# Performance work log

Measured on AMD Instinct MI355X. Metric: run time of the kernel, lower is better.

The kernel has to match this reference:

```python
import jax, jax.numpy as jnp
import numpy as np
import math

B, S, U, H = 8, 1024, 1024, 16
DK = U // H  # 64


def setup_inputs() -> dict:
    key = jax.random.key(0)
    ks = jax.random.split(key, 12)
    query = jax.random.normal(ks[0], (B, S, U), jnp.float32)
    key_t = jax.random.normal(ks[1], (B, S, U), jnp.float32)  # unused by module (bug preserved)
    value = jax.random.normal(ks[2], (B, S, U), jnp.float32)  # unused by module (bug preserved)
    # causal multiplicative 0/1 mask [B,S,S]
    mask = jnp.broadcast_to(jnp.tril(jnp.ones((S, S), jnp.float32)), (B, S, S))
    bh = math.sqrt(1.0 / DK)   # init bound for per-head projections (out_features=d_k)
    bo = math.sqrt(1.0 / U)    # init bound for output projection (out_features=n_units)
    u = lambda k, shape, b: jax.random.uniform(k, shape, jnp.float32, -b, b)
    # per-head weights stacked: [H, U, DK] (already input->output layout)
    Wq = u(ks[3], (H, U, DK), bh); bq = u(ks[4], (H, DK), bh)
    Wk = u(ks[5], (H, U, DK), bh); bk = u(ks[6], (H, DK), bh)
    Wv = u(ks[7], (H, U, DK), bh); bv = u(ks[8], (H, DK), bh)
    Wo = u(ks[9], (U, U), bo);     bo_ = u(ks[10], (U,), bo)
    return dict(query=query, key=key_t, value=value, mask=mask,
                Wq=Wq, bq=bq, Wk=Wk, bk=bk, Wv=Wv, bv=bv, Wo=Wo, bo=bo_)


def reference(query, key, value, mask, Wq, bq, Wk, bk, Wv, bv, Wo, bo):
    # NOTE: faithful to source — q, k, v are ALL projected from `query`.
    q = jnp.einsum('bsu,hud->bhsd', query, Wq) + bq[:, None, :]
    k = jnp.einsum('bsu,hud->bhsd', query, Wk) + bk[:, None, :]
    v = jnp.einsum('bsu,hud->bhsd', query, Wv) + bv[:, None, :]
    scores = jnp.einsum('bhqd,bhkd->bhqk', q, k) / math.sqrt(DK)
    s = mask[:, None, :, :]  # broadcast over heads
    x = scores * s - 1e9 * (1.0 - s)  # multiplicative mask baked into softmax input
    attn = jax.nn.softmax(x, axis=-1)
    out = jnp.einsum('bhqk,bhkd->bhqd', attn, v)
    # concat heads along feature dim (head 0 first, matching torch.cat order)
    out = out.transpose(0, 2, 1, 3).reshape(B, S, U)
    return out @ Wo + bo
```

## Files before the change

### kernel.cpp

```cpp
#include <hip/hip_runtime.h>
#include <hip/hip_bf16.h>

#define B_ 8
#define S_ 1024
#define U_ 1024
#define H_ 16
#define DK_ 64

typedef __attribute__((ext_vector_type(8))) short short8;
typedef __attribute__((ext_vector_type(4))) float f32x4;
typedef __attribute__((ext_vector_type(16))) float f32x16;

__device__ inline ushort f2b(float x) {
  union { float f; unsigned u; } v; v.f = x;
  unsigned r = (v.u + 0x7FFFu + ((v.u >> 16) & 1u)) >> 16;
  return (ushort)r;
}
__device__ inline unsigned pk2(float lo, float hi) {
  return (unsigned)f2b(lo) | ((unsigned)f2b(hi) << 16);
}

__device__ inline void gld16(const ushort* g, ushort* l) {
  __builtin_amdgcn_global_load_lds((__attribute__((address_space(1))) void*)(g),
                                   (__attribute__((address_space(3))) void*)(l),
                                   16, 0, 0);
}

__global__ __launch_bounds__(256) void pack_all_kern(
    const float* __restrict__ X, ushort* __restrict__ Xb,
    const float* __restrict__ Wq, const float* __restrict__ Wk, const float* __restrict__ Wv,
    const float* __restrict__ bq, const float* __restrict__ bk, const float* __restrict__ bv,
    const float* __restrict__ Wo,
    ushort* __restrict__ Wqkv, float* __restrict__ Bqkv, ushort* __restrict__ Wob)
{
  __shared__ ushort tile[64*65];
  const int t = threadIdx.x;
  if (blockIdx.x < 4096) {
    int idx = blockIdx.x * 256 + t;
    const float4* src = (const float4*)X + (size_t)idx * 2;
    float4 a = src[0], b = src[1];
    ushort r[8];
    r[0]=f2b(a.x); r[1]=f2b(a.y); r[2]=f2b(a.z); r[3]=f2b(a.w);
    r[4]=f2b(b.x); r[5]=f2b(b.y); r[6]=f2b(b.z); r[7]=f2b(b.w);
    *(uint4*)(Xb + (size_t)idx*8) = *(uint4*)r;
    return;
  }
  const int bid = blockIdx.x - 4096;
  if (bid < 768) {
    int p = bid >> 8, rem = bid & 255;
    int h = rem >> 4, kc = rem & 15, k0 = kc*64;
    const float* Wsrc = (p==0) ? Wq : ((p==1) ? Wk : Wv);
    #pragma unroll
    for (int i = 0; i < 16; ++i) {
      int e = t + i*256;
      int r = e >> 6, d = e & 63;
      tile[d*65 + r] = f2b(Wsrc[h*65536 + (k0+r)*64 + d]);
    }
    __syncthreads();
    #pragma unroll
    for (int i = 0; i < 16; ++i) {
      int e = t + i*256;
      int d = e >> 6, r = e & 63;
      Wqkv[(size_t)(p*1024 + h*64 + d)*1024 + k0 + r] = tile[d*65 + r];
    }
    if (kc == 0 && t < 64) {
      const float* bsrc = (p==0) ? bq : ((p==1) ? bk : bv);
      Bqkv[p*1024 + h*64 + t] = bsrc[h*64 + t];
    }
  } else {
    int b2 = bid - 768;
    int nc = b2 >> 4, kc = b2 & 15;
    int n0 = nc*64, k0 = kc*64;
    #pragma unroll
    for (int i = 0; i < 16; ++i) {
      int e = t + i*256;
      int r = e >> 6, d = e & 63;
      tile[d*65 + r] = f2b(Wo[(size_t)(k0+r)*1024 + n0 + d]);
    }
    __syncthreads();
    #pragma unroll
    for (int i = 0; i < 16; ++i) {
      int e = t + i*256;
      int d = e >> 6, r = e & 63;
      Wob[(size_t)(n0+d)*1024 + k0 + r] = tile[d*65 + r];
    }
  }
}

template<int MODE>
__global__ __launch_bounds__(256, 3) void gemm128_kern(
    const ushort* __restrict__ A,
    const ushort* __restrict__ Bw,
    const float* __restrict__ bias,
    ushort* __restrict__ Qb, ushort* __restrict__ Kb, ushort* __restrict__ Vtb,
    float* __restrict__ outF)
{
  __shared__ __align__(16) ushort As[3][4096];
  __shared__ __align__(16) ushort Bs[3][4096];

  const int t = threadIdx.x;
  const int l = t & 63, w = t >> 6;
  const int wr = w >> 1, wc = w & 1;
  const int li = l & 15, c4 = l >> 4;

  int m0, n0;
  if (MODE==0) {
    int swz = (blockIdx.x & 7) * 192 + (blockIdx.x >> 3);
    int ms = swz / 192, rem = swz % 192;
    m0 = (ms*8 + (rem & 7)) * 128;  n0 = (rem >> 3) * 128;
  } else {
    int swz = (blockIdx.x & 7) * 64 + (blockIdx.x >> 3);
    int ms = swz / 64, rem = swz % 64;
    m0 = (ms*8 + (rem & 7)) * 128;  n0 = (rem >> 3) * 128;
  }

  f32x4 acc[4][4];
  #pragma unroll
  for (int i=0;i<4;i++)
    #pragma unroll
    for (int j=0;j<4;j++) acc[i][j] = (f32x4)0.0f;

  auto SA = [&](int buf, int kk) {
    #pragma unroll
    for (int p2=0;p2<2;++p2) {
      int n = p2*256 + t;
      int row = n >> 2, jj = (n & 3) ^ ((row >> 1) & 3);
      gld16(&A[(size_t)(m0 + row)*1024 + kk + jj*8], &As[buf][n*8]);
    }
  };
  auto SB = [&](int buf, int kk) {
    #pragma unroll
    for (int p2=0;p2<2;++p2) {
      int n = p2*256 + t;
      int row = n >> 2, jj = (n & 3) ^ ((row >> 1) & 3);
      gld16(&Bw[(size_t)(n0 + row)*1024 + kk + jj*8], &Bs[buf][n*8]);
    }
  };

  SA(0, 0);  SB(0, 0);
  SA(1, 32); SB(1, 32);

  for (int kt = 0; kt < 32; ++kt) {
    const int cur = kt % 3;
    asm volatile("s_waitcnt vmcnt(4)" ::: "memory");
    __builtin_amdgcn_s_barrier();
    __builtin_amdgcn_sched_barrier(0);

    short8 af[4], bf[4];
    #pragma unroll
    for (int i=0;i<4;i++) {
      int rA = wr*64 + i*16 + li;
      int rB = wc*64 + i*16 + li;
      af[i] = *(const short8*)&As[cur][rA*32 + ((c4 ^ ((rA>>1)&3))*8)];
      bf[i] = *(const short8*)&Bs[cur][rB*32 + ((c4 ^ ((rB>>1)&3))*8)];
    }
    __builtin_amdgcn_s_barrier();
    __builtin_amdgcn_sched_barrier(0);
    const int nb = (kt + 2) % 3;
    const int kk2 = ((kt + 2) & 31) * 32;
    SA(nb, kk2); SB(nb, kk2);

    __builtin_amdgcn_s_setprio(1);
    #pragma unroll
    for (int i=0;i<4;i++)
      #pragma unroll
      for (int j=0;j<4;j++)
        acc[i][j] = __builtin_amdgcn_mfma_f32_16x16x32_bf16(af[i], bf[j], acc[i][j], 0,0,0);
    __builtin_amdgcn_s_setprio(0);
  }

  #pragma unroll
  for (int i=0;i<4;i++) {
    int rbase = m0 + wr*64 + i*16 + c4*4;
    #pragma unroll
    for (int j=0;j<4;j++) {
      int col = n0 + wc*64 + j*16 + li;
      float bv = bias[col];
      if (MODE == 0) {
        int p = col >> 10, h = (col >> 6) & 15, d = col & 63;
        int b = rbase >> 10, s = rbase & 1023;
        if (p == 2) {
          ushort pk4[4];
          #pragma unroll
          for (int r=0;r<4;r++) pk4[r] = f2b(acc[i][j][r] + bv);
          *(uint2*)&Vtb[((size_t)((b*16+h)*64 + d))*1024 + s] = *(uint2*)pk4;
        } else {
          ushort* dst = (p==0) ? Qb : Kb;
          float sc = (p==0) ? 0.18033688011112042f : 1.0f;
          #pragma unroll
          for (int r=0;r<4;r++)
            dst[(((size_t)(b*16 + h))*1024 + s + r)*64 + d] = f2b((acc[i][j][r] + bv) * sc);
        }
      } else {
        #pragma unroll
        for (int r=0;r<4;r++)
          outF[(size_t)(rbase+r)*1024 + col] = acc[i][j][r] + bv;
      }
    }
  }
}

__global__ __launch_bounds__(256, 2) void attn_kern(
    const ushort* __restrict__ Qb, const ushort* __restrict__ Kb,
    const ushort* __restrict__ Vt, ushort* __restrict__ Ob)
{
  __shared__ __align__(16) ushort Pb[4][32*40];
  __shared__ __align__(16) ushort OT[4][32*72];
  const int t = threadIdx.x, l = t & 63, w = t >> 6;
  const int bid = blockIdx.x;
  const int x = bid & 7, i0 = bid >> 3;
  const int bh = x*16 + (i0 >> 2);
  const int p  = (i0 & 3)*4 + w;
  const int qta = p, qtb = 31 - p;

  const int col = l & 31, hi = l >> 5;
  const ushort* Qp = Qb + (size_t)bh*65536;
  const ushort* Kp = Kb + (size_t)bh*65536;
  const ushort* Vp = Vt + (size_t)bh*65536;

  short8 qfa[4], qfb[4];
  #pragma unroll
  for (int m=0;m<4;m++) {
    qfa[m] = *(const short8*)&Qp[(size_t)(qta*32+col)*64 + m*16 + hi*8];
    qfb[m] = *(const short8*)&Qp[(size_t)(qtb*32+col)*64 + m*16 + hi*8];
  }

  f32x16 aA0 = (f32x16)0.0f, aA1 = (f32x16)0.0f;
  f32x16 aB0 = (f32x16)0.0f, aB1 = (f32x16)0.0f;
  float mA = -1e30f, lA = 0.0f, mB = -1e30f, lB = 0.0f;
  ushort* Pw = &Pb[w][0];

  auto PROC = [&](f32x16& s, bool diag, float& mR, float& lS,
                  f32x16& o0, f32x16& o1, const short8* vf0, const short8* vf1) {
    if (diag) {
      #pragma unroll
      for (int r=0;r<16;r++) {
        int kvl = (r&3) + ((r>>2)<<3) + 4*hi;
        s[r] = (kvl > col) ? -1e9f : s[r];
      }
    }
    float mx = s[0];
    #pragma unroll
    for (int r=1;r<16;r++) mx = fmaxf(mx, s[r]);
    mx = fmaxf(mx, __shfl_xor(mx, 32));
    if (__any(mx - mR > 8.0f)) {
      float mN = fmaxf(mR, mx);
      float corr = __builtin_amdgcn_exp2f(mR - mN);
      mR = mN; lS *= corr;
      #pragma unroll
      for (int r=0;r<16;r++) { o0[r] *= corr; o1[r] *= corr; }
    }
    float pr[16], rs = 0.0f;
    #pragma unroll
    for (int r=0;r<16;r++) { pr[r] = __builtin_amdgcn_exp2f(s[r] - mR); rs += pr[r]; }
    rs += __shfl_xor(rs, 32);
    lS += rs;
    #pragma unroll
    for (int r2=0;r2<8;r2++) {
      int r = 2*r2;
      int kv = (r&3) + ((r>>2)<<3) + 4*hi;
      *(unsigned*)&Pw[col*40 + kv] = pk2(pr[r], pr[r+1]);
    }
    short8 pb0 = *(const short8*)&Pw[col*40 + hi*8];
    short8 pb1 = *(const short8*)&Pw[col*40 + 16 + hi*8];
    o0 = __builtin_amdgcn_mfma_f32_32x32x16_bf16(vf0[0], pb0, o0, 0,0,0);
    o0 = __builtin_amdgcn_mfma_f32_32x32x16_bf16(vf0[1], pb1, o0, 0,0,0);
    o1 = __builtin_amdgcn_mfma_f32_32x32x16_bf16(vf1[0], pb0, o1, 0,0,0);
    o1 = __builtin_amdgcn_mfma_f32_32x32x16_bf16(vf1[1], pb1, o1, 0,0,0);
  };

  auto LOADKV = [&](int kt, short8* kf_, short8* v0_, short8* v1_) {
    #pragma unroll
    for (int m=0;m<4;m++)
      kf_[m] = *(const short8*)&Kp[(size_t)(kt*32+col)*64 + m*16 + hi*8];
    #pragma unroll
    for (int m=0;m<2;m++) {
      v0_[m] = *(const short8*)&Vp[(size_t)col*1024      + kt*32 + m*16 + hi*8];
      v1_[m] = *(const short8*)&Vp[(size_t)(32+col)*1024 + kt*32 + m*16 + hi*8];
    }
  };

  short8 kf[4], vf0[2], vf1[2];
  LOADKV(0, kf, vf0, vf1);

  for (int kt = 0; kt <= qtb; ++kt) {
    short8 kf2[4], v02[2], v12[2];
    const int ktn = (kt + 1 <= qtb) ? kt + 1 : qtb;
    LOADKV(ktn, kf2, v02, v12);

    const bool doA = (kt <= qta);
    f32x16 sB = (f32x16)0.0f, sA = (f32x16)0.0f;
    #pragma unroll
    for (int m=0;m<4;m++)
      sB = __builtin_amdgcn_mfma_f32_32x32x16_bf16(kf[m], qfb[m], sB, 0, 0, 0);
    if (doA) {
      #pragma unroll
      for (int m=0;m<4;m++)
        sA = __builtin_amdgcn_mfma_f32_32x32x16_bf16(kf[m], qfa[m], sA, 0, 0, 0);
    }

    PROC(sB, kt == qtb, mB, lB, aB0, aB1, vf0, vf1);
    if (doA) PROC(sA, kt == qta, mA, lA, aA0, aA1, vf0, vf1);

    #pragma unroll
    for (int m=0;m<4;m++) kf[m] = kf2[m];
    #pragma unroll
    for (int m=0;m<2;m++) { vf0[m] = v02[m]; vf1[m] = v12[m]; }
  }

  const int b = bh >> 4, h = bh & 15;
  auto EPI = [&](int qt, float lS, const f32x16& o0, const f32x16& o1) {
    float inv = 1.0f / lS;
    ushort* o = &OT[w][0];
    #pragma unroll
    for (int r2=0;r2<8;r2++) {
      int r = 2*r2;
      int dv = (r&3) + ((r>>2)<<3) + 4*hi;
      *(unsigned*)&o[col*72 + dv]      = pk2(o0[r]*inv, o0[r+1]*inv);
      *(unsigned*)&o[col*72 + 32 + dv] = pk2(o1[r]*inv, o1[r+1]*inv);
    }
    #pragma unroll
    for (int it=0; it<4; ++it) {
      int q = it*8 + (l>>3), c8 = (l&7)*8;
      uint4 v = *(const uint4*)&o[q*72 + c8];
      int qg = qt*32 + q;
      *(uint4*)&Ob[(size_t)(b*1024+qg)*1024 + h*64 + c8] = v;
    }
  };
  EPI(qta, lA, aA0, aA1);
  EPI(qtb, lB, aB0, aB1);
}

extern "C" void kernel_launch(void* const* d_in, const int* in_sizes, int n_in,
                              void* d_out, int out_size, void* d_ws, size_t ws_size,
                              hipStream_t stream) {
  const float* query = (const float*)d_in[0];
  const float* Wq = (const float*)d_in[4];
  const float* bq = (const float*)d_in[5];
  const float* Wk = (const float*)d_in[6];
  const float* bk = (const float*)d_in[7];
  const float* Wv = (const float*)d_in[8];
  const float* bv = (const float*)d_in[9];
  const float* Wo = (const float*)d_in[10];
  const float* bo = (const float*)d_in[11];

  char* wsb = (char*)d_ws;
  ushort* Xb   = (ushort*)(wsb);
  ushort* Wqkv = (ushort*)(wsb + 16777216);
  float*  Bqkv = (float*) (wsb + 23068672);
  ushort* Wob  = (ushort*)(wsb + 23080960);
  ushort* Qb   = (ushort*)(wsb + 25178112);
  ushort* Kb   = (ushort*)(wsb + 41955328);
  ushort* Vtb  = (ushort*)(wsb + 58732544);
  ushort* Ob   = (ushort*)(wsb + 75509760);

  hipLaunchKernelGGL(pack_all_kern, dim3(5120), dim3(256), 0, stream,
                     query, Xb, Wq, Wk, Wv, bq, bk, bv, Wo, Wqkv, Bqkv, Wob);
  hipLaunchKernelGGL(gemm128_kern<0>, dim3(1536), dim3(256), 0, stream,
                     Xb, Wqkv, Bqkv, Qb, Kb, Vtb, (float*)nullptr);
  hipLaunchKernelGGL(attn_kern, dim3(512), dim3(256), 0, stream, Qb, Kb, Vtb, Ob);
  hipLaunchKernelGGL(gemm128_kern<1>, dim3(512), dim3(256), 0, stream,
                     Ob, Wob, bo, (ushort*)nullptr, (ushort*)nullptr, (ushort*)nullptr,
                     (float*)d_out);
}
```

Before: 164.4 us.

## Share K/V tiles across waves via double-buffered LDS in attention kernel

Before, each of the four waves loaded its own K and V fragments straight from global memory. Now the block loads each 32-key K/V tile once into double-buffered shared memory, prefetching the next tile into registers, and every wave reads its fragments from there. The loop runs to the longest wave's tile count, with per-wave predication and a block barrier every iteration. Max and sum reductions are also rewritten as trees to shorten dependency chains. The cost is idle waves at the barrier, because query ranges differ per wave, plus extra shared memory that may lower occupancy.

```diff
diff --git a/kernel.cpp b/kernel.cpp
--- a/kernel.cpp
+++ b/kernel.cpp
@@ -204,19 +204,26 @@
     const ushort* __restrict__ Qb, const ushort* __restrict__ Kb,
     const ushort* __restrict__ Vt, ushort* __restrict__ Ob)
 {
+  __shared__ __align__(16) ushort Ks[2][32*68];
+  __shared__ __align__(16) ushort Vs[2][64*44];
   __shared__ __align__(16) ushort Pb[4][32*40];
   __shared__ __align__(16) ushort OT[4][32*72];
   const int t = threadIdx.x, l = t & 63, w = t >> 6;
   const int bid = blockIdx.x;
   const int x = bid & 7, i0 = bid >> 3;
   const int bh = x*16 + (i0 >> 2);
-  const int p  = (i0 & 3)*4 + w;
+  const int g  = i0 & 3;
+  const int p  = g*4 + w;
   const int qta = p, qtb = 31 - p;
+  const int NT = 32 - g*4;
 
   const int col = l & 31, hi = l >> 5;
   const ushort* Qp = Qb + (size_t)bh*65536;
   const ushort* Kp = Kb + (size_t)bh*65536;
   const ushort* Vp = Vt + (size_t)bh*65536;
+
+  const int ks_row = t >> 3, ks_c = t & 7;
+  const int vs_row = t >> 2, vs_c = t & 3;
 
   short8 qfa[4], qfb[4];
   #pragma unroll
@@ -239,9 +246,12 @@
         s[r] = (kvl > col) ? -1e9f : s[r];
       }
     }
-    float mx = s[0];
-    #pragma unroll
-    for (int r=1;r<16;r++) mx = fmaxf(mx, s[r]);
+    float m8[8];
+    #pragma unroll
+    for (int r2=0;r2<8;r2++) m8[r2] = fmaxf(s[2*r2], s[2*r2+1]);
+    #pragma unroll
+    for (int r2=0;r2<4;r2++) m8[r2] = fmaxf(m8[r2], m8[r2+4]);
+    float mx = fmaxf(fmaxf(m8[0],m8[1]), fmaxf(m8[2],m8[3]));
     mx = fmaxf(mx, __shfl_xor(mx, 32));
     if (__any(mx - mR > 8.0f)) {
       float mN = fmaxf(mR, mx);
@@ -250,9 +260,15 @@
       #pragma unroll
       for (int r=0;r<16;r++) { o0[r] *= corr; o1[r] *= corr; }
     }
-    float pr[16], rs = 0.0f;
-    #pragma unroll
-    for (int r=0;r<16;r++) { pr[r] = __builtin_amdgcn_exp2f(s[r] - mR); rs += pr[r]; }
+    float pr[16];
+    #pragma unroll
+    for (int r=0;r<16;r++) pr[r] = __builtin_amdgcn_exp2f(s[r] - mR);
+    float s8[8];
+    #pragma unroll
+    for (int r2=0;r2<8;r2++) s8[r2] = pr[2*r2] + pr[2*r2+1];
+    #pragma unroll
+    for (int r2=0;r2<4;r2++) s8[r2] += s8[r2+4];
+    float rs = (s8[0]+s8[1]) + (s8[2]+s8[3]);
     rs += __shfl_xor(rs, 32);
     lS += rs;
     #pragma unroll
@@ -269,43 +285,56 @@
     o1 = __builtin_amdgcn_mfma_f32_32x32x16_bf16(vf1[1], pb1, o1, 0,0,0);
   };
 
-  auto LOADKV = [&](int kt, short8* kf_, short8* v0_, short8* v1_) {
+  {
+    uint4 k0v = *(const uint4*)&Kp[(size_t)ks_row*64 + ks_c*8];
+    uint4 v0v = *(const uint4*)&Vp[(size_t)vs_row*1024 + vs_c*8];
+    *(uint4*)&Ks[0][ks_row*68 + ks_c*8] = k0v;
+    *(uint4*)&Vs[0][vs_row*44 + vs_c*8] = v0v;
+  }
+  __syncthreads();
+
+  for (int kt = 0; kt < NT; ++kt) {
+    const int cur = kt & 1;
+    const bool pre = (kt + 1 < NT);
+    uint4 kn2, vn2;
+    if (pre) {
+      kn2 = *(const uint4*)&Kp[(size_t)((kt+1)*32+ks_row)*64 + ks_c*8];
+      vn2 = *(const uint4*)&Vp[(size_t)vs_row*1024 + (kt+1)*32 + vs_c*8];
+    }
+
+    short8 kf[4], vf0[2], vf1[2];
     #pragma unroll
     for (int m=0;m<4;m++)
-      kf_[m] = *(const short8*)&Kp[(size_t)(kt*32+col)*64 + m*16 + hi*8];
+      kf[m] = *(const short8*)&Ks[cur][col*68 + m*16 + hi*8];
     #pragma unroll
     for (int m=0;m<2;m++) {
-      v0_[m] = *(const short8*)&Vp[(size_t)col*1024      + kt*32 + m*16 + hi*8];
-      v1_[m] = *(const short8*)&Vp[(size_t)(32+col)*1024 + kt*32 + m*16 + hi*8];
-    }
-  };
-
-  short8 kf[4], vf0[2], vf1[2];
-  LOADKV(0, kf, vf0, vf1);
-
-  for (int kt = 0; kt <= qtb; ++kt) {
-    short8 kf2[4], v02[2], v12[2];
-    const int ktn = (kt + 1 <= qtb) ? kt + 1 : qtb;
-    LOADKV(ktn, kf2, v02, v12);
-
-    const bool doA = (kt <= qta);
-    f32x16 sB = (f32x16)0.0f, sA = (f32x16)0.0f;
-    #pragma unroll
-    for (int m=0;m<4;m++)
-      sB = __builtin_amdgcn_mfma_f32_32x32x16_bf16(kf[m], qfb[m], sB, 0, 0, 0);
-    if (doA) {
+      vf0[m] = *(const short8*)&Vs[cur][col*44 + m*16 + hi*8];
+      vf1[m] = *(const short8*)&Vs[cur][(col+32)*44 + m*16 + hi*8];
+    }
+
+    const bool doB = (kt <= qtb), doA = (kt <= qta);
+    if (doB) {
+      f32x16 sB = (f32x16)0.0f;
       #pragma unroll
       for (int m=0;m<4;m++)
-        sA = __builtin_amdgcn_mfma_f32_32x32x16_bf16(kf[m], qfa[m], sA, 0, 0, 0);
-    }
-
-    PROC(sB, kt == qtb, mB, lB, aB0, aB1, vf0, vf1);
-    if (doA) PROC(sA, kt == qta, mA, lA, aA0, aA1, vf0, vf1);
-
-    #pragma unroll
-    for (int m=0;m<4;m++) kf[m] = kf2[m];
-    #pragma unroll
-    for (int m=0;m<2;m++) { vf0[m] = v02[m]; vf1[m] = v12[m]; }
+        sB = __builtin_amdgcn_mfma_f32_32x32x16_bf16(kf[m], qfb[m], sB, 0, 0, 0);
+      if (doA) {
+        f32x16 sA = (f32x16)0.0f;
+        #pragma unroll
+        for (int m=0;m<4;m++)
+          sA = __builtin_amdgcn_mfma_f32_32x32x16_bf16(kf[m], qfa[m], sA, 0, 0, 0);
+        PROC(sB, kt == qtb, mB, lB, aB0, aB1, vf0, vf1);
+        PROC(sA, kt == qta, mA, lA, aA0, aA1, vf0, vf1);
+      } else {
+        PROC(sB, kt == qtb, mB, lB, aB0, aB1, vf0, vf1);
+      }
+    }
+
+    if (pre) {
+      *(uint4*)&Ks[cur^1][ks_row*68 + ks_c*8] = kn2;
+      *(uint4*)&Vs[cur^1][vs_row*44 + vs_c*8] = vn2;
+    }
+    __syncthreads();
   }
 
   const int b = bh >> 4, h = bh & 15;
```

After: 152.7 us. 1.08x faster.
